# Optimization experiments

Hardware: AMD Instinct MI355X
Metric: run time of the kernel (lower is better)

The kernel has to match this reference:

```python
import jax, jax.numpy as jnp
import numpy as np

B_, L, HID = 2, 1024, 2048
N, H, P, NA = 128, 64, 64, 32   # state, heads, head_dim, rope angle pairs
DIN = 2 * H * P + 2 * N + 3 * H + NA  # 8672
EPS = 1e-5
A_FLOOR = 1e-4


def setup_inputs() -> dict:
    key = jax.random.key(0)
    k0, k1, k2 = jax.random.split(key, 3)
    hidden_states = jax.random.normal(k0, (B_, L, HID), jnp.float32)
    in_proj_w = jax.random.normal(k1, (DIN, HID), jnp.float32) * 0.02
    out_proj_w = jax.random.normal(k2, (HID, H * P), jnp.float32) * 0.02
    # dt_bias init exactly as in the torch module
    rng = np.random.default_rng(0)
    dt = np.exp(rng.random(H) * (np.log(0.1) - np.log(0.001)) + np.log(0.001))
    dt = np.clip(dt, 1e-4, None)
    dt_bias = jnp.asarray(dt + np.log(-np.expm1(-dt)), jnp.float32)
    return {
        'hidden_states': hidden_states,
        'in_proj_w': in_proj_w,
        'dt_bias': dt_bias,
        'B_bias': jnp.ones((H, N), jnp.float32),
        'C_bias': jnp.ones((H, N), jnp.float32),
        'B_norm_w': jnp.ones((N,), jnp.float32),
        'C_norm_w': jnp.ones((N,), jnp.float32),
        'D': jnp.ones((H,), jnp.float32),
        'out_proj_w': out_proj_w,
    }


def _rmsnorm(x, w):
    var = jnp.mean(jnp.square(x), axis=-1, keepdims=True)
    return x * jax.lax.rsqrt(var + EPS) * w


def _forward(hidden_states, in_proj_w, dt_bias, B_bias, C_bias,
             B_norm_w, C_norm_w, D, out_proj_w):
    b, l, _ = hidden_states.shape
    proj = hidden_states @ in_proj_w.T  # (b,l,DIN)
    splits = np.cumsum([H * P, H * P, N, N, H, H, H])
    z, x, Braw, Craw, dd_dt, dd_A, trap, angles = jnp.split(proj, splits, axis=-1)
    z = z.reshape(b, l, H, P)
    x = x.reshape(b, l, H, P)
    # data-dependent A (per token, per head), clamped
    A = jnp.minimum(-jax.nn.softplus(dd_A.astype(jnp.float32)), -A_FLOOR)
    DT = jax.nn.softplus(dd_dt + dt_bias)          # (b,l,H)
    decay = jnp.exp(A * DT)                        # (b,l,H)
    lam = jax.nn.sigmoid(trap)                     # trapezoidal weight (b,l,H)
    # RMSNorm then per-head input-independent bias (n_groups=1, mimo_rank=1)
    Bn = _rmsnorm(Braw, B_norm_w)[:, :, None, :] + B_bias  # (b,l,H,N)
    Cn = _rmsnorm(Craw, C_norm_w)[:, :, None, :] + C_bias  # (b,l,H,N)
    # blockwise rotary on first 2*NA state dims, cumulative data-dependent phase
    phase = jnp.cumsum(angles[:, :, None, :].astype(jnp.float32) * DT[..., None], axis=1)  # (b,l,H,NA)
    cos, sin = jnp.cos(phase), jnp.sin(phase)

    def rope(v):
        v1, v2, rest = v[..., :NA], v[..., NA:2 * NA], v[..., 2 * NA:]
        return jnp.concatenate([v1 * cos - v2 * sin, v1 * sin + v2 * cos, rest], axis=-1)

    Bh = rope(Bn.astype(jnp.float32))
    Ch = rope(Cn.astype(jnp.float32))
    u = (x * DT[..., None]).astype(jnp.float32)    # (b,l,H,P)

    # selective scan with generalized trapezoidal discretization:
    # h_t = a_t h_{t-1} + (1-lam_t) u_t B_t^T + lam_t a_t u_{t-1} B_{t-1}^T
    def step(carry, inp):
        h, Gp = carry
        Bt, Ct, ut, dec, lm = inp
        G = ut[..., :, None] * Bt[..., None, :]    # (b,H,P,N)
        h = dec[..., None, None] * h + (1.0 - lm)[..., None, None] * G \
            + (lm * dec)[..., None, None] * Gp
        y = jnp.einsum('bhpn,bhn->bhp', h, Ct)
        return (h, G), y

    h0 = jnp.zeros((b, H, P, N), jnp.float32)
    xs = (Bh.transpose(1, 0, 2, 3), Ch.transpose(1, 0, 2, 3),
          u.transpose(1, 0, 2, 3), decay.transpose(1, 0, 2), lam.transpose(1, 0, 2))
    _, ys = jax.lax.scan(step, (h0, h0), xs)       # (l,b,H,P)
    y = ys.transpose(1, 0, 2, 3)
    y = y + D[None, None, :, None] * x             # skip connection
    y = y * jax.nn.silu(z)                         # output gate (Z path in kernel)
    y = y.reshape(b, l, H * P)
    return y @ out_proj_w.T


def reference(hidden_states, in_proj_w, dt_bias, B_bias, C_bias,
              B_norm_w, C_norm_w, D, out_proj_w):
    return _forward(hidden_states, in_proj_w, dt_bias, B_bias, C_bias,
                    B_norm_w, C_norm_w, D, out_proj_w)
```

## Files before the change

### kernel.cpp

```cpp
#include <hip/hip_runtime.h>
#include <hip/hip_bf16.h>
#include <cstdint>
#include <cstddef>

#define DEVINL __device__ __forceinline__

typedef __attribute__((ext_vector_type(8))) short bf16x8;
typedef __attribute__((ext_vector_type(4))) float f32x4;

DEVINL float bf2f(unsigned short u){
  union { unsigned u32; float f; } cv; cv.u32 = ((unsigned)u) << 16; return cv.f;
}
DEVINL unsigned short f2bf(float f){
  union { float f; unsigned u32; } cv; cv.f = f;
  unsigned u = cv.u32;
  return (unsigned short)((u + 0x7FFFu + ((u >> 16) & 1u)) >> 16);
}
DEVINL float softplusf(float x){ return x > 20.f ? x : log1pf(expf(x)); }

DEVINL void g2l16(const void* gptr, void* ldsptr){
  __builtin_amdgcn_global_load_lds(
      (const __attribute__((address_space(1))) unsigned int*)gptr,
      (__attribute__((address_space(3))) unsigned int*)(uintptr_t)ldsptr,
      16, 0, 0);
}

DEVINL int swzb(int row, int col){ return row*256 + ((col*2) ^ ((row&7)<<4)); }
DEVINL void ldsw_write8(unsigned short* b, int row, int col, bf16x8 v){
  *(bf16x8*)((char*)b + swzb(row,col)) = v;
}
DEVINL bf16x8 ldsw_read8(const unsigned short* b, int row, int col){
  return *(const bf16x8*)((const char*)b + swzb(row,col));
}
DEVINL void ldsw_write1(unsigned short* b, int row, int col, unsigned short v){
  *(unsigned short*)((char*)b + swzb(row,col)) = v;
}
DEVINL unsigned short ldsw_read1(const unsigned short* b, int row, int col){
  return *(const unsigned short*)((const char*)b + swzb(row,col));
}

__global__ __launch_bounds__(256) void k_conv2(
    const float* __restrict__ a, unsigned short* __restrict__ oa, long na, int nba,
    const float* __restrict__ b, unsigned short* __restrict__ ob, long nb)
{
  const float* in; unsigned short* out; long n; long blk;
  if ((int)blockIdx.x < nba){ in = a; out = oa; n = na; blk = blockIdx.x; }
  else                      { in = b; out = ob; n = nb; blk = blockIdx.x - nba; }
  long i = (blk * 256 + threadIdx.x) * 4;
  if (i + 3 < n){
    float4 v = *(const float4*)(in + i);
    unsigned long long pk =
        (unsigned long long)f2bf(v.x)
      | ((unsigned long long)f2bf(v.y) << 16)
      | ((unsigned long long)f2bf(v.z) << 32)
      | ((unsigned long long)f2bf(v.w) << 48);
    *(unsigned long long*)(out + i) = pk;
  }
}

__global__ __launch_bounds__(256) void k_f32_to_bf16(
    const float* __restrict__ in, unsigned short* __restrict__ out, long n)
{
  long i = ((long)blockIdx.x * 256 + threadIdx.x) * 4;
  if (i + 3 < n){
    float4 v = *(const float4*)(in + i);
    unsigned long long pk =
        (unsigned long long)f2bf(v.x)
      | ((unsigned long long)f2bf(v.y) << 16)
      | ((unsigned long long)f2bf(v.z) << 32)
      | ((unsigned long long)f2bf(v.w) << 48);
    *(unsigned long long*)(out + i) = pk;
  }
}

template<bool OUT_BF16>
__global__ __launch_bounds__(256) void k_gemm_bt(
    const unsigned short* __restrict__ A,
    const unsigned short* __restrict__ Bt,
    void* __restrict__ Cout,
    int K, int Nrows, int Npad, int xm, int tmx, int tnx)
{
  __shared__ unsigned short Asub[128*64];
  __shared__ unsigned short Bsub[128*64];
  const int tid = threadIdx.x;
  const int x = blockIdx.x & 7, i = blockIdx.x >> 3;
  const int rt = (x % xm) * tmx + (i % tmx);
  const int ct = (x / xm) * tnx + (i / tmx);
  const int lane = tid & 63, wave = tid >> 6;
  const int wr = wave >> 1, wc = wave & 1;
  const int fr = lane & 15;
  const int fq = lane >> 4;

  const int srow0 = tid >> 3;
  const int sgrp  = (tid & 7) ^ ((tid >> 3) & 7);
  size_t aoff[4], boff[4];
  #pragma unroll
  for (int j = 0; j < 4; j++){
    int row = j*32 + srow0;
    aoff[j] = (size_t)(rt*128 + row) * K + sgrp*8;
    int brow = ct*128 + row; if (brow > Nrows-1) brow = Nrows-1;
    boff[j] = (size_t)brow * K + sgrp*8;
  }

  f32x4 acc[4][4] = {};

  for (int k0 = 0; k0 < K; k0 += 64){
    #pragma unroll
    for (int j = 0; j < 4; j++){
      g2l16(A  + aoff[j] + k0, (char*)Asub + (j*256 + tid)*16);
      g2l16(Bt + boff[j] + k0, (char*)Bsub + (j*256 + tid)*16);
    }
    asm volatile("s_waitcnt vmcnt(0)" ::: "memory");
    __syncthreads();

    #pragma unroll
    for (int kk = 0; kk < 2; kk++){
      bf16x8 af[4], bfr[4];
      const int slot = (kk*4 + fq) ^ (fr & 7);
      #pragma unroll
      for (int j = 0; j < 4; j++){
        int ra = wr*64 + j*16 + fr;
        int rb = wc*64 + j*16 + fr;
        af[j]  = *(const bf16x8*)((const char*)Asub + ra*128 + slot*16);
        bfr[j] = *(const bf16x8*)((const char*)Bsub + rb*128 + slot*16);
      }
      #pragma unroll
      for (int mi = 0; mi < 4; mi++)
        #pragma unroll
        for (int ni = 0; ni < 4; ni++)
          acc[mi][ni] = __builtin_amdgcn_mfma_f32_16x16x32_bf16(af[mi], bfr[ni], acc[mi][ni], 0, 0, 0);
    }
    __syncthreads();
  }

  const int er = (lane >> 4) * 4;
  const int ec = lane & 15;
  #pragma unroll
  for (int mi = 0; mi < 4; mi++){
    #pragma unroll
    for (int ni = 0; ni < 4; ni++){
      const int row = rt*128 + wr*64 + mi*16 + er;
      const int col = ct*128 + wc*64 + ni*16 + ec;
      #pragma unroll
      for (int r = 0; r < 4; r++){
        if (OUT_BF16)
          ((unsigned short*)Cout)[(size_t)(row+r)*Npad + col] = f2bf(acc[mi][ni][r]);
        else
          ((float*)Cout)[(size_t)(row+r)*Npad + col] = acc[mi][ni][r];
      }
    }
  }
}

__global__ __launch_bounds__(128) void k_rmsprep(
    const unsigned short* __restrict__ proj, const float* __restrict__ Bw,
    const float* __restrict__ Cw, const float* __restrict__ dt_bias,
    unsigned short* __restrict__ Bb2, unsigned short* __restrict__ Cb2,
    float* __restrict__ DTt, float* __restrict__ logdec, float* __restrict__ lamt)
{
  int row = blockIdx.x, n = threadIdx.x;
  size_t base = (size_t)row * 8704;
  float bv = bf2f(proj[base + 8192 + n]);
  float cv = bf2f(proj[base + 8320 + n]);
  float sb = bv*bv, sc = cv*cv;
  #pragma unroll
  for (int m = 1; m < 64; m <<= 1){ sb += __shfl_xor(sb, m, 64); sc += __shfl_xor(sc, m, 64); }
  __shared__ float red[4];
  if ((n & 63) == 0){ red[(n>>6)*2] = sb; red[(n>>6)*2+1] = sc; }
  __syncthreads();
  sb = red[0] + red[2];
  sc = red[1] + red[3];
  float rb = rsqrtf(sb*(1.f/128.f) + 1e-5f);
  float rc = rsqrtf(sc*(1.f/128.f) + 1e-5f);
  Bb2[row*128 + n] = f2bf(bv*rb*Bw[n]);
  Cb2[row*128 + n] = f2bf(cv*rc*Cw[n]);
  if (n < 64){
    int h = n, b = row >> 10, l = row & 1023;
    float dd_dt = bf2f(proj[base + 8448 + h]);
    float dd_A  = bf2f(proj[base + 8512 + h]);
    float trap  = bf2f(proj[base + 8576 + h]);
    float DT = softplusf(dd_dt + dt_bias[h]);
    float A  = -fmaxf(softplusf(dd_A), 1e-4f);
    size_t o = ((size_t)(b*64 + h))*1024 + l;
    DTt[o]    = DT;
    logdec[o] = A * DT;
    lamt[o]   = 1.f / (1.f + expf(-trap));
  }
}

__global__ __launch_bounds__(256) void k_phase(
    const unsigned short* __restrict__ proj, const float* __restrict__ DTt,
    const float* __restrict__ logdec, const float* __restrict__ lamt,
    float* __restrict__ clcb, float* __restrict__ gb,
    unsigned short* __restrict__ cosb, unsigned short* __restrict__ sinb)
{
  int bh = blockIdx.x, b = bh >> 6, h = bh & 63;
  int tid = threadIdx.x;
  size_t sbase = (size_t)bh * 1024;
  {
    int e0 = tid * 4;
    float v0 = logdec[sbase+e0], v1 = logdec[sbase+e0+1],
          v2 = logdec[sbase+e0+2], v3 = logdec[sbase+e0+3];
    float p0 = v0, p1 = p0+v1, p2 = p1+v2, p3 = p2+v3;
    float tot = p3;
    int sub = tid & 31;
    float incl = tot;
    #pragma unroll
    for (int off = 1; off < 32; off <<= 1){
      float u = __shfl_up(incl, off, 32);
      if (sub >= off) incl += u;
    }
    float excl = incl - tot;
    clcb[sbase+e0]   = excl + p0;
    clcb[sbase+e0+1] = excl + p1;
    clcb[sbase+e0+2] = excl + p2;
    clcb[sbase+e0+3] = excl + p3;
    #pragma unroll
    for (int q = 0; q < 4; q++){
      int l = e0 + q;
      int ln = (l == 1023) ? 1023 : l + 1;
      gb[sbase+l] = 1.f - lamt[sbase+l] + lamt[sbase+ln];
    }
  }
  int na = tid & 31, c = tid >> 5;
  __shared__ float part[8][32];
  const float* dtr = DTt + sbase;
  float s = 0.f;
  for (int q = 0; q < 128; q++){
    int l = c*128 + q; int row = b*1024 + l;
    float ang = bf2f(proj[(size_t)row*8704 + 8640 + na]);
    s = fmaf(ang, dtr[l], s);
  }
  part[c][na] = s;
  __syncthreads();
  float off = 0.f;
  for (int cc = 0; cc < c; cc++) off += part[cc][na];
  float ph = off;
  for (int q = 0; q < 128; q++){
    int l = c*128 + q; int row = b*1024 + l;
    float ang = bf2f(proj[(size_t)row*8704 + 8640 + na]);
    ph = fmaf(ang, dtr[l], ph);
    float sn, cs;
    __sincosf(ph, &sn, &cs);
    size_t o = ((size_t)row*64 + h)*32 + na;
    cosb[o] = f2bf(cs); sinb[o] = f2bf(sn);
  }
}

__global__ __launch_bounds__(512, 1) void k_intra(
    const unsigned short* __restrict__ proj,
    const unsigned short* __restrict__ Bb2, const unsigned short* __restrict__ Cb2,
    const float* __restrict__ Bbias, const float* __restrict__ Cbias,
    const unsigned short* __restrict__ cosb, const unsigned short* __restrict__ sinb,
    const float* __restrict__ DTt, const float* __restrict__ clcb,
    const float* __restrict__ gb, const float* __restrict__ lamt,
    const float* __restrict__ Dv, unsigned short* __restrict__ ybf,
    unsigned short* __restrict__ Gbuf)
{
  const int c = blockIdx.x & 7, bh = blockIdx.x >> 3;
  const int b = bh >> 6, h = bh & 63;
  const int tid = threadIdx.x, lane = tid & 63, wave = tid >> 6;
  const int wr = wave >> 2, wc = wave & 3;
  const int fr = lane & 15, fq = lane >> 4;

  __shared__ __align__(16) unsigned short Cs[128*128];
  __shared__ __align__(16) unsigned short Bs[128*128];
  __shared__ __align__(16) unsigned short BTs[128*128];
  __shared__ __align__(16) unsigned short Uts[64*128];
  __shared__ float clcs[128], lams[128], gs[128], wUs[128], dts[128];
  __shared__ float biasB[128], biasC[128];

  const int base = b*1024 + c*128;
  const size_t shbase = (size_t)bh * 1024;
  const float Dh = Dv[h];

  if (tid < 128){
    int l = c*128 + tid;
    clcs[tid] = clcb[shbase + l];
    dts[tid]  = DTt[shbase + l];
    lams[tid] = lamt[shbase + l];
    gs[tid]   = gb[shbase + l];
    biasB[tid] = Bbias[h*128 + tid];
  } else if (tid < 256){
    biasC[tid-128] = Cbias[h*128 + tid-128];
  }
  __syncthreads();
  if (tid < 128) wUs[tid] = __expf(clcs[127] - clcs[tid]) * gs[tid];

  {
    const int t = tid >> 2, q = tid & 3;
    const int grow = base + t;
    const size_t roff = (size_t)grow*128;
    if (q == 0){
      bf16x8 cc[4], sv[4];
      #pragma unroll
      for (int j = 0; j < 4; j++){
        cc[j] = *(const bf16x8*)(cosb + ((size_t)grow*64 + h)*32 + j*8);
        sv[j] = *(const bf16x8*)(sinb + ((size_t)grow*64 + h)*32 + j*8);
      }
      #pragma unroll
      for (int j = 0; j < 4; j++){
        bf16x8 vlo = *(const bf16x8*)(Cb2 + roff + j*8);
        bf16x8 vhi = *(const bf16x8*)(Cb2 + roff + 32 + j*8);
        bf16x8 olo, ohi;
        #pragma unroll
        for (int e = 0; e < 8; e++){
          float a = bf2f((unsigned short)vlo[e]) + biasC[j*8+e];
          float d = bf2f((unsigned short)vhi[e]) + biasC[32+j*8+e];
          float cf = bf2f((unsigned short)cc[j][e]);
          float sf = bf2f((unsigned short)sv[j][e]);
          olo[e] = (short)f2bf(a*cf - d*sf);
          ohi[e] = (short)f2bf(a*sf + d*cf);
        }
        ldsw_write8(Cs, t, j*8, olo);
        ldsw_write8(Cs, t, 32 + j*8, ohi);
      }
    } else if (q == 1){
      #pragma unroll
      for (int j = 0; j < 8; j++){
        bf16x8 v = *(const bf16x8*)(Cb2 + roff + 64 + j*8);
        bf16x8 o;
        #pragma unroll
        for (int e = 0; e < 8; e++) o[e] = (short)f2bf(bf2f((unsigned short)v[e]) + biasC[64+j*8+e]);
        ldsw_write8(Cs, t, 64 + j*8, o);
      }
    } else if (q == 2){
      bf16x8 cc[4], sv[4];
      #pragma unroll
      for (int j = 0; j < 4; j++){
        cc[j] = *(const bf16x8*)(cosb + ((size_t)grow*64 + h)*32 + j*8);
        sv[j] = *(const bf16x8*)(sinb + ((size_t)grow*64 + h)*32 + j*8);
      }
      #pragma unroll
      for (int j = 0; j < 4; j++){
        bf16x8 vlo = *(const bf16x8*)(Bb2 + roff + j*8);
        bf16x8 vhi = *(const bf16x8*)(Bb2 + roff + 32 + j*8);
        bf16x8 olo, ohi;
        #pragma unroll
        for (int e = 0; e < 8; e++){
          float a = bf2f((unsigned short)vlo[e]) + biasB[j*8+e];
          float d = bf2f((unsigned short)vhi[e]) + biasB[32+j*8+e];
          float cf = bf2f((unsigned short)cc[j][e]);
          float sf = bf2f((unsigned short)sv[j][e]);
          olo[e] = (short)f2bf(a*cf - d*sf);
          ohi[e] = (short)f2bf(a*sf + d*cf);
        }
        ldsw_write8(Bs, t, j*8, olo);
        ldsw_write8(Bs, t, 32 + j*8, ohi);
        #pragma unroll
        for (int e = 0; e < 8; e++){
          ldsw_write1(BTs, j*8+e, t, (unsigned short)olo[e]);
          ldsw_write1(BTs, 32+j*8+e, t, (unsigned short)ohi[e]);
        }
      }
    } else {
      #pragma unroll
      for (int j = 0; j < 8; j++){
        bf16x8 v = *(const bf16x8*)(Bb2 + roff + 64 + j*8);
        bf16x8 o;
        #pragma unroll
        for (int e = 0; e < 8; e++) o[e] = (short)f2bf(bf2f((unsigned short)v[e]) + biasB[64+j*8+e]);
        ldsw_write8(Bs, t, 64 + j*8, o);
        #pragma unroll
        for (int e = 0; e < 8; e++) ldsw_write1(BTs, 64+j*8+e, t, (unsigned short)o[e]);
      }
    }
  }
  {
    const int p = tid & 63, jg = tid >> 6;
    #pragma unroll 4
    for (int q = 0; q < 16; q++){
      int j = jg*16 + q;
      size_t pb = (size_t)(base + j) * 8704;
      float xx = bf2f(proj[pb + 4096 + h*64 + p]);
      ldsw_write1(Uts, p, j, f2bf(xx * dts[j]));
    }
  }
  __syncthreads();

  f32x4 acc1[4][2];
  #pragma unroll
  for (int mi = 0; mi < 4; mi++)
    #pragma unroll
    for (int ni = 0; ni < 2; ni++)
      acc1[mi][ni] = (f32x4){0.f,0.f,0.f,0.f};
  #pragma unroll
  for (int ks = 0; ks < 4; ks++){
    bf16x8 af[4], bj[2];
    #pragma unroll
    for (int mi = 0; mi < 4; mi++) af[mi] = ldsw_read8(Cs, wr*64+mi*16+fr, ks*32+fq*8);
    #pragma unroll
    for (int ni = 0; ni < 2; ni++) bj[ni] = ldsw_read8(Bs, wc*32+ni*16+fr, ks*32+fq*8);
    #pragma unroll
    for (int mi = 0; mi < 4; mi++)
      #pragma unroll
      for (int ni = 0; ni < 2; ni++)
        acc1[mi][ni] = __builtin_amdgcn_mfma_f32_16x16x32_bf16(af[mi], bj[ni], acc1[mi][ni], 0,0,0);
  }
  unsigned short pr[4][2][4];
  int jj[2]; float clcj[2], gj[2];
  #pragma unroll
  for (int ni = 0; ni < 2; ni++){ jj[ni] = wc*32+ni*16+fr; clcj[ni] = clcs[jj[ni]]; gj[ni] = gs[jj[ni]]; }
  #pragma unroll
  for (int mi = 0; mi < 4; mi++){
    #pragma unroll
    for (int r = 0; r < 4; r++){
      int t = wr*64+mi*16+fq*4+r;
      float ct_ = clcs[t], lt = lams[t];
      #pragma unroll
      for (int ni = 0; ni < 2; ni++){
        int j = jj[ni];
        float w = (j < t) ? __expf(ct_ - clcj[ni])*gj[ni] : ((j == t) ? (1.f - lt) : 0.f);
        pr[mi][ni][r] = f2bf(acc1[mi][ni][r] * w);
      }
    }
  }
  __syncthreads();
  #pragma unroll
  for (int mi = 0; mi < 4; mi++)
    #pragma unroll
    for (int ni = 0; ni < 2; ni++)
      #pragma unroll
      for (int r = 0; r < 4; r++)
        ldsw_write1(Bs, wr*64+mi*16+fq*4+r, wc*32+ni*16+fr, pr[mi][ni][r]);
  __syncthreads();

  f32x4 acc2[4];
  #pragma unroll
  for (int mi = 0; mi < 4; mi++) acc2[mi] = (f32x4){0.f,0.f,0.f,0.f};
  #pragma unroll
  for (int ks = 0; ks < 4; ks++){
    bf16x8 af[4], uj;
    #pragma unroll
    for (int mi = 0; mi < 4; mi++) af[mi] = ldsw_read8(Bs, wr*64+mi*16+fr, ks*32+fq*8);
    uj = ldsw_read8(Uts, wc*16+fr, ks*32+fq*8);
    #pragma unroll
    for (int mi = 0; mi < 4; mi++)
      acc2[mi] = __builtin_amdgcn_mfma_f32_16x16x32_bf16(af[mi], uj, acc2[mi], 0,0,0);
  }
  f32x4 accS[2][2];
  #pragma unroll
  for (int mi = 0; mi < 2; mi++)
    #pragma unroll
    for (int ni = 0; ni < 2; ni++)
      accS[mi][ni] = (f32x4){0.f,0.f,0.f,0.f};
  #pragma unroll
  for (int ks = 0; ks < 4; ks++){
    bf16x8 au[2], bn[2];
    #pragma unroll
    for (int mi = 0; mi < 2; mi++){
      bf16x8 raw = ldsw_read8(Uts, wr*32+mi*16+fr, ks*32+fq*8);
      #pragma unroll
      for (int e = 0; e < 8; e++){
        float f = bf2f((unsigned short)raw[e]) * wUs[ks*32+fq*8+e];
        au[mi][e] = (short)f2bf(f);
      }
    }
    #pragma unroll
    for (int ni = 0; ni < 2; ni++) bn[ni] = ldsw_read8(BTs, wc*32+ni*16+fr, ks*32+fq*8);
    #pragma unroll
    for (int mi = 0; mi < 2; mi++)
      #pragma unroll
      for (int ni = 0; ni < 2; ni++)
        accS[mi][ni] = __builtin_amdgcn_mfma_f32_16x16x32_bf16(au[mi], bn[ni], accS[mi][ni], 0,0,0);
  }

  #pragma unroll
  for (int mi = 0; mi < 4; mi++){
    #pragma unroll
    for (int r = 0; r < 4; r++){
      int t = wr*64+mi*16+fq*4+r;
      int p = wc*16+fr;
      float xv = bf2f(ldsw_read1(Uts, p, t)) / fmaxf(dts[t], 1e-30f);
      float o = acc2[mi][r] + Dh*xv;
      ybf[(size_t)(base + t)*4096 + h*64 + p] = f2bf(o);
    }
  }
  #pragma unroll
  for (int mi = 0; mi < 2; mi++)
    #pragma unroll
    for (int ni = 0; ni < 2; ni++)
      #pragma unroll
      for (int r = 0; r < 4; r++){
        int p = wr*32+mi*16+fq*4+r;
        int n = wc*32+ni*16+fr;
        Gbuf[(size_t)blockIdx.x*8192 + p*128 + n] = f2bf(accS[mi][ni][r]);
      }
}

__global__ __launch_bounds__(256) void k_scanstate(
    const float* __restrict__ clcb, unsigned short* __restrict__ Gbuf)
{
  const int bh = blockIdx.x, tid = threadIdx.x;
  float S[32];
  #pragma unroll
  for (int q = 0; q < 32; q++) S[q] = 0.f;
  const size_t gbase = (size_t)bh*65536 + (size_t)tid*32;
  for (int c = 0; c < 8; c++){
    float decEnd = __expf(clcb[(size_t)bh*1024 + c*128 + 127]);
    unsigned short* p = Gbuf + gbase + (size_t)c*8192;
    bf16x8 g[4], s[4];
    #pragma unroll
    for (int q = 0; q < 4; q++) g[q] = *(const bf16x8*)(p + q*8);
    #pragma unroll
    for (int q = 0; q < 4; q++)
      #pragma unroll
      for (int e = 0; e < 8; e++) s[q][e] = (short)f2bf(S[q*8+e]);
    #pragma unroll
    for (int q = 0; q < 4; q++) *(bf16x8*)(p + q*8) = s[q];
    #pragma unroll
    for (int q = 0; q < 4; q++)
      #pragma unroll
      for (int e = 0; e < 8; e++)
        S[q*8+e] = decEnd*S[q*8+e] + bf2f((unsigned short)g[q][e]);
  }
}

__global__ __launch_bounds__(256) void k_inter(
    const unsigned short* __restrict__ proj,
    const unsigned short* __restrict__ Cb2, const float* __restrict__ Cbias,
    const unsigned short* __restrict__ cosb, const unsigned short* __restrict__ sinb,
    const float* __restrict__ clcb, const unsigned short* __restrict__ Sprev,
    unsigned short* __restrict__ ybf)
{
  const int c = blockIdx.x & 7, bh = blockIdx.x >> 3;
  const int b = bh >> 6, h = bh & 63;
  const int tid = threadIdx.x, lane = tid & 63, wave = tid >> 6;
  const int wr = wave >> 1, wc = wave & 1;
  const int fr = lane & 15, fq = lane >> 4;

  __shared__ __align__(16) unsigned short Cs[128*128];
  __shared__ __align__(16) unsigned short Ss[64*128];
  __shared__ float expclcs[128], biasC[128];

  const int base = b*1024 + c*128;

  if (tid < 128){
    expclcs[tid] = __expf(clcb[(size_t)bh*1024 + c*128 + tid]);
    biasC[tid] = Cbias[h*128 + tid];
  }
  __syncthreads();

  {
    const int t = tid >> 1, half = tid & 1;
    const int grow = base + t;
    const size_t roff = (size_t)grow*128 + half*64;
    if (half == 0){
      bf16x8 cc[4], sv[4];
      #pragma unroll
      for (int j = 0; j < 4; j++){
        cc[j] = *(const bf16x8*)(cosb + ((size_t)grow*64 + h)*32 + j*8);
        sv[j] = *(const bf16x8*)(sinb + ((size_t)grow*64 + h)*32 + j*8);
      }
      #pragma unroll
      for (int j = 0; j < 4; j++){
        bf16x8 vlo = *(const bf16x8*)(Cb2 + roff + j*8);
        bf16x8 vhi = *(const bf16x8*)(Cb2 + roff + 32 + j*8);
        bf16x8 olo, ohi;
        #pragma unroll
        for (int e = 0; e < 8; e++){
          float a = bf2f((unsigned short)vlo[e]) + biasC[j*8+e];
          float d = bf2f((unsigned short)vhi[e]) + biasC[32+j*8+e];
          float cf = bf2f((unsigned short)cc[j][e]);
          float sf = bf2f((unsigned short)sv[j][e]);
          olo[e] = (short)f2bf(a*cf - d*sf);
          ohi[e] = (short)f2bf(a*sf + d*cf);
        }
        ldsw_write8(Cs, t, j*8, olo);
        ldsw_write8(Cs, t, 32 + j*8, ohi);
      }
    } else {
      #pragma unroll
      for (int j = 0; j < 8; j++){
        bf16x8 v = *(const bf16x8*)(Cb2 + roff + j*8);
        bf16x8 o;
        #pragma unroll
        for (int e = 0; e < 8; e++) o[e] = (short)f2bf(bf2f((unsigned short)v[e]) + biasC[64+j*8+e]);
        ldsw_write8(Cs, t, 64 + j*8, o);
      }
    }
  }
  {
    const unsigned short* src = Sprev + (size_t)blockIdx.x*8192 + (size_t)tid*32;
    #pragma unroll
    for (int j = 0; j < 4; j++){
      bf16x8 v = *(const bf16x8*)(src + j*8);
      int f = tid*32 + j*8;
      ldsw_write8(Ss, f >> 7, f & 127, v);
    }
  }
  __syncthreads();

  f32x4 acc[4][2];
  #pragma unroll
  for (int mi = 0; mi < 4; mi++)
    #pragma unroll
    for (int ni = 0; ni < 2; ni++)
      acc[mi][ni] = (f32x4){0.f,0.f,0.f,0.f};
  #pragma unroll
  for (int ks = 0; ks < 4; ks++){
    bf16x8 af[4], sj[2];
    #pragma unroll
    for (int mi = 0; mi < 4; mi++) af[mi] = ldsw_read8(Cs, wr*64+mi*16+fr, ks*32+fq*8);
    #pragma unroll
    for (int ni = 0; ni < 2; ni++) sj[ni] = ldsw_read8(Ss, wc*32+ni*16+fr, ks*32+fq*8);
    #pragma unroll
    for (int mi = 0; mi < 4; mi++)
      #pragma unroll
      for (int ni = 0; ni < 2; ni++)
        acc[mi][ni] = __builtin_amdgcn_mfma_f32_16x16x32_bf16(af[mi], sj[ni], acc[mi][ni], 0,0,0);
  }

  #pragma unroll
  for (int mi = 0; mi < 4; mi++){
    #pragma unroll
    for (int ni = 0; ni < 2; ni++){
      #pragma unroll
      for (int r = 0; r < 4; r++){
        int t = wr*64+mi*16+fq*4+r;
        int p = wc*32+ni*16+fr;
        size_t yoff = (size_t)(base + t)*4096 + h*64 + p;
        float y = bf2f(ybf[yoff]) + expclcs[t]*acc[mi][ni][r];
        float zv = bf2f(proj[(size_t)(base + t)*8704 + h*64 + p]);
        float sl = zv / (1.f + __expf(-zv));
        ybf[yoff] = f2bf(y * sl);
      }
    }
  }
}

extern "C" void kernel_launch(void* const* d_in, const int* in_sizes, int n_in,
                              void* d_out, int out_size, void* d_ws, size_t ws_size,
                              hipStream_t stream)
{
  const float* hs    = (const float*)d_in[0];
  const float* w1    = (const float*)d_in[1];
  const float* dtb   = (const float*)d_in[2];
  const float* Bbias = (const float*)d_in[3];
  const float* Cbias = (const float*)d_in[4];
  const float* Bw    = (const float*)d_in[5];
  const float* Cw    = (const float*)d_in[6];
  const float* Dv    = (const float*)d_in[7];
  const float* wo    = (const float*)d_in[8];
  float* out = (float*)d_out;
  char* ws = (char*)d_ws;

  unsigned short* projbf = (unsigned short*)(ws + 0UL);
  unsigned short* W1bf   = (unsigned short*)(ws + 35651584UL);
  unsigned short* Gbuf   = W1bf;
  unsigned short* Wobf   = W1bf;
  unsigned short* ybf    = (unsigned short*)(ws + 52428800UL);
  unsigned short* hsbf   = (unsigned short*)(ws + 71172096UL);
  unsigned short* cosb   = hsbf;
  unsigned short* sinb   = (unsigned short*)(ws + 79560704UL);
  float* DTt    = (float*)(ws + 87949312UL);
  float* logdec = (float*)(ws + 88473600UL);
  float* lamt   = (float*)(ws + 88997888UL);
  float* clcb   = (float*)(ws + 89522176UL);
  float* gb     = (float*)(ws + 90046464UL);
  unsigned short* Bb2 = (unsigned short*)(ws + 90570752UL);
  unsigned short* Cb2 = (unsigned short*)(ws + 91095040UL);
  if (ws_size < 91619328UL) return;

  (void)in_sizes; (void)n_in; (void)out_size;

  k_conv2<<<21440, 256, 0, stream>>>(w1, W1bf, 17760256L, 17344, hs, hsbf, 4194304L);
  k_gemm_bt<true><<<1088, 256, 0, stream>>>(hsbf, W1bf, projbf, 2048, 8672, 8704, 2, 8, 17);
  k_rmsprep<<<2048, 128, 0, stream>>>(projbf, Bw, Cw, dtb, Bb2, Cb2, DTt, logdec, lamt);
  k_phase<<<128, 256, 0, stream>>>(projbf, DTt, logdec, lamt, clcb, gb, cosb, sinb);
  k_intra<<<1024, 512, 0, stream>>>(projbf, Bb2, Cb2, Bbias, Cbias,
                                    cosb, sinb, DTt, clcb, gb, lamt, Dv, ybf, Gbuf);
  k_scanstate<<<128, 256, 0, stream>>>(clcb, Gbuf);
  k_inter<<<1024, 256, 0, stream>>>(projbf, Cb2, Cbias, cosb, sinb, clcb, Gbuf, ybf);
  k_f32_to_bf16<<<8192, 256, 0, stream>>>(wo, Wobf, 8388608L);
  k_gemm_bt<false><<<256, 256, 0, stream>>>(ybf, Wobf, out, 4096, 2048, 2048, 4, 4, 8);
}
```

Baseline: 332.7 us.

## Fuse rmsnorm prep into phase kernel and fold out_proj weight conversion into input cast

Merges the per-row RMSNorm/gating prep and the per-head scan/phase kernel into a single launch. Head blocks compute DT, log-decay and lambda directly into shared memory, which removes the logdec round trip through global memory. When the workspace is large enough, the out_proj weight fp32->bf16 conversion moves into the first conversion launch using a separate buffer, dropping a late kernel launch. The head blocks now do strided gathers from proj for their own timesteps, and the larger-workspace path depends on how much workspace the harness provides.

```diff
diff --git a/kernel.cpp b/kernel.cpp
--- a/kernel.cpp
+++ b/kernel.cpp
@@ -39,13 +39,15 @@
   return *(const unsigned short*)((const char*)b + swzb(row,col));
 }
 
-__global__ __launch_bounds__(256) void k_conv2(
+__global__ __launch_bounds__(256) void k_conv3(
     const float* __restrict__ a, unsigned short* __restrict__ oa, long na, int nba,
-    const float* __restrict__ b, unsigned short* __restrict__ ob, long nb)
+    const float* __restrict__ b, unsigned short* __restrict__ ob, long nb, int nbb,
+    const float* __restrict__ c, unsigned short* __restrict__ oc, long nc)
 {
   const float* in; unsigned short* out; long n; long blk;
-  if ((int)blockIdx.x < nba){ in = a; out = oa; n = na; blk = blockIdx.x; }
-  else                      { in = b; out = ob; n = nb; blk = blockIdx.x - nba; }
+  if ((int)blockIdx.x < nba)            { in = a; out = oa; n = na; blk = blockIdx.x; }
+  else if ((int)blockIdx.x < nba + nbb) { in = b; out = ob; n = nb; blk = blockIdx.x - nba; }
+  else                                  { in = c; out = oc; n = nc; blk = blockIdx.x - nba - nbb; }
   long i = (blk * 256 + threadIdx.x) * 4;
   if (i + 3 < n){
     float4 v = *(const float4*)(in + i);
@@ -152,55 +154,60 @@
   }
 }
 
-__global__ __launch_bounds__(128) void k_rmsprep(
+__global__ __launch_bounds__(256) void k_prep(
     const unsigned short* __restrict__ proj, const float* __restrict__ Bw,
-    const float* __restrict__ Cw, const float* __restrict__ dt_bias,
+    const float* __restrict__ Cw, const float* __restrict__ dtb,
     unsigned short* __restrict__ Bb2, unsigned short* __restrict__ Cb2,
-    float* __restrict__ DTt, float* __restrict__ logdec, float* __restrict__ lamt)
-{
-  int row = blockIdx.x, n = threadIdx.x;
-  size_t base = (size_t)row * 8704;
-  float bv = bf2f(proj[base + 8192 + n]);
-  float cv = bf2f(proj[base + 8320 + n]);
-  float sb = bv*bv, sc = cv*cv;
-  #pragma unroll
-  for (int m = 1; m < 64; m <<= 1){ sb += __shfl_xor(sb, m, 64); sc += __shfl_xor(sc, m, 64); }
-  __shared__ float red[4];
-  if ((n & 63) == 0){ red[(n>>6)*2] = sb; red[(n>>6)*2+1] = sc; }
-  __syncthreads();
-  sb = red[0] + red[2];
-  sc = red[1] + red[3];
-  float rb = rsqrtf(sb*(1.f/128.f) + 1e-5f);
-  float rc = rsqrtf(sc*(1.f/128.f) + 1e-5f);
-  Bb2[row*128 + n] = f2bf(bv*rb*Bw[n]);
-  Cb2[row*128 + n] = f2bf(cv*rc*Cw[n]);
-  if (n < 64){
-    int h = n, b = row >> 10, l = row & 1023;
-    float dd_dt = bf2f(proj[base + 8448 + h]);
-    float dd_A  = bf2f(proj[base + 8512 + h]);
-    float trap  = bf2f(proj[base + 8576 + h]);
-    float DT = softplusf(dd_dt + dt_bias[h]);
-    float A  = -fmaxf(softplusf(dd_A), 1e-4f);
-    size_t o = ((size_t)(b*64 + h))*1024 + l;
-    DTt[o]    = DT;
-    logdec[o] = A * DT;
-    lamt[o]   = 1.f / (1.f + expf(-trap));
-  }
-}
-
-__global__ __launch_bounds__(256) void k_phase(
-    const unsigned short* __restrict__ proj, const float* __restrict__ DTt,
-    const float* __restrict__ logdec, const float* __restrict__ lamt,
+    float* __restrict__ DTt, float* __restrict__ lamt,
     float* __restrict__ clcb, float* __restrict__ gb,
     unsigned short* __restrict__ cosb, unsigned short* __restrict__ sinb)
 {
-  int bh = blockIdx.x, b = bh >> 6, h = bh & 63;
-  int tid = threadIdx.x;
-  size_t sbase = (size_t)bh * 1024;
+  const int tid = threadIdx.x;
+  __shared__ float dtL[1024], ldL[1024], lamL[1024];
+  __shared__ float part[8][32];
+  __shared__ float red[8];
+
+  if (blockIdx.x >= 128){
+    int row = (int)(blockIdx.x - 128)*2 + (tid >> 7);
+    int n = tid & 127;
+    size_t base = (size_t)row * 8704;
+    float bv = bf2f(proj[base + 8192 + n]);
+    float cv = bf2f(proj[base + 8320 + n]);
+    float sb = bv*bv, sc = cv*cv;
+    #pragma unroll
+    for (int m = 1; m < 64; m <<= 1){ sb += __shfl_xor(sb, m, 64); sc += __shfl_xor(sc, m, 64); }
+    int w = tid >> 6;
+    if ((tid & 63) == 0){ red[w*2] = sb; red[w*2+1] = sc; }
+    __syncthreads();
+    int rw = (tid >> 7) * 2;
+    sb = red[rw*2]   + red[rw*2+2];
+    sc = red[rw*2+1] + red[rw*2+3];
+    float rb = rsqrtf(sb*(1.f/128.f) + 1e-5f);
+    float rc = rsqrtf(sc*(1.f/128.f) + 1e-5f);
+    Bb2[row*128 + n] = f2bf(bv*rb*Bw[n]);
+    Cb2[row*128 + n] = f2bf(cv*rc*Cw[n]);
+    return;
+  }
+
+  const int bh = blockIdx.x, b = bh >> 6, h = bh & 63;
+  const size_t sbase = (size_t)bh * 1024;
+  #pragma unroll
+  for (int q = 0; q < 4; q++){
+    int l = tid*4 + q;
+    size_t pb = (size_t)(b*1024 + l) * 8704;
+    float dd_dt = bf2f(proj[pb + 8448 + h]);
+    float dd_A  = bf2f(proj[pb + 8512 + h]);
+    float trap  = bf2f(proj[pb + 8576 + h]);
+    float DT  = softplusf(dd_dt + dtb[h]);
+    float A   = -fmaxf(softplusf(dd_A), 1e-4f);
+    float lam = 1.f / (1.f + expf(-trap));
+    dtL[l] = DT; ldL[l] = A*DT; lamL[l] = lam;
+    DTt[sbase+l] = DT; lamt[sbase+l] = lam;
+  }
+  __syncthreads();
   {
     int e0 = tid * 4;
-    float v0 = logdec[sbase+e0], v1 = logdec[sbase+e0+1],
-          v2 = logdec[sbase+e0+2], v3 = logdec[sbase+e0+3];
+    float v0 = ldL[e0], v1 = ldL[e0+1], v2 = ldL[e0+2], v3 = ldL[e0+3];
     float p0 = v0, p1 = p0+v1, p2 = p1+v2, p3 = p2+v3;
     float tot = p3;
     int sub = tid & 31;
@@ -219,17 +226,15 @@
     for (int q = 0; q < 4; q++){
       int l = e0 + q;
       int ln = (l == 1023) ? 1023 : l + 1;
-      gb[sbase+l] = 1.f - lamt[sbase+l] + lamt[sbase+ln];
+      gb[sbase+l] = 1.f - lamL[l] + lamL[ln];
     }
   }
   int na = tid & 31, c = tid >> 5;
-  __shared__ float part[8][32];
-  const float* dtr = DTt + sbase;
   float s = 0.f;
   for (int q = 0; q < 128; q++){
     int l = c*128 + q; int row = b*1024 + l;
     float ang = bf2f(proj[(size_t)row*8704 + 8640 + na]);
-    s = fmaf(ang, dtr[l], s);
+    s = fmaf(ang, dtL[l], s);
   }
   part[c][na] = s;
   __syncthreads();
@@ -239,7 +244,7 @@
   for (int q = 0; q < 128; q++){
     int l = c*128 + q; int row = b*1024 + l;
     float ang = bf2f(proj[(size_t)row*8704 + 8640 + na]);
-    ph = fmaf(ang, dtr[l], ph);
+    ph = fmaf(ang, dtL[l], ph);
     float sn, cs;
     __sincosf(ph, &sn, &cs);
     size_t o = ((size_t)row*64 + h)*32 + na;
@@ -648,13 +653,11 @@
   unsigned short* projbf = (unsigned short*)(ws + 0UL);
   unsigned short* W1bf   = (unsigned short*)(ws + 35651584UL);
   unsigned short* Gbuf   = W1bf;
-  unsigned short* Wobf   = W1bf;
   unsigned short* ybf    = (unsigned short*)(ws + 52428800UL);
   unsigned short* hsbf   = (unsigned short*)(ws + 71172096UL);
   unsigned short* cosb   = hsbf;
   unsigned short* sinb   = (unsigned short*)(ws + 79560704UL);
   float* DTt    = (float*)(ws + 87949312UL);
-  float* logdec = (float*)(ws + 88473600UL);
   float* lamt   = (float*)(ws + 88997888UL);
   float* clcb   = (float*)(ws + 89522176UL);
   float* gb     = (float*)(ws + 90046464UL);
@@ -662,16 +665,21 @@
   unsigned short* Cb2 = (unsigned short*)(ws + 91095040UL);
   if (ws_size < 91619328UL) return;
 
+  const bool bigws = (ws_size >= 91619328UL + 16777216UL);
+  unsigned short* Wobf = bigws ? (unsigned short*)(ws + 91619328UL) : W1bf;
+
   (void)in_sizes; (void)n_in; (void)out_size;
 
-  k_conv2<<<21440, 256, 0, stream>>>(w1, W1bf, 17760256L, 17344, hs, hsbf, 4194304L);
+  k_conv3<<<bigws ? 29632 : 21440, 256, 0, stream>>>(
+      w1, W1bf, 17760256L, 17344, hs, hsbf, 4194304L, 4096, wo, Wobf, 8388608L);
   k_gemm_bt<true><<<1088, 256, 0, stream>>>(hsbf, W1bf, projbf, 2048, 8672, 8704, 2, 8, 17);
-  k_rmsprep<<<2048, 128, 0, stream>>>(projbf, Bw, Cw, dtb, Bb2, Cb2, DTt, logdec, lamt);
-  k_phase<<<128, 256, 0, stream>>>(projbf, DTt, logdec, lamt, clcb, gb, cosb, sinb);
+  k_prep<<<1152, 256, 0, stream>>>(projbf, Bw, Cw, dtb, Bb2, Cb2,
+                                   DTt, lamt, clcb, gb, cosb, sinb);
   k_intra<<<1024, 512, 0, stream>>>(projbf, Bb2, Cb2, Bbias, Cbias,
                                     cosb, sinb, DTt, clcb, gb, lamt, Dv, ybf, Gbuf);
   k_scanstate<<<128, 256, 0, stream>>>(clcb, Gbuf);
   k_inter<<<1024, 256, 0, stream>>>(projbf, Cb2, Cbias, cosb, sinb, clcb, Gbuf, ybf);
-  k_f32_to_bf16<<<8192, 256, 0, stream>>>(wo, Wobf, 8388608L);
+  if (!bigws)
+    k_f32_to_bf16<<<8192, 256, 0, stream>>>(wo, Wobf, 8388608L);
   k_gemm_bt<false><<<256, 256, 0, stream>>>(ybf, Wobf, out, 4096, 2048, 2048, 4, 4, 8);
 }
```

Result: faster. 324.3 us (-2.5%).
